# Performance work log

Measured on AMD Instinct MI355X. Metric: run time of the kernel, lower is better.

The kernel has to match this reference:

```python
import jax, jax.numpy as jnp
import numpy as np
import math

K = 4          # wavelet polynomial order
C = 16         # channel multiplier
MODES = 64     # retained Fourier modes (alpha)
L_LEVEL = 0    # coarsest level
B_SZ, N_SZ = 32, 8192
CK = C * K


def _get_filter_legendre(k):
    """Pure-numpy port of get_filter(base='legendre', k): Alpert multiwavelet filters."""
    from numpy.polynomial import legendre as npleg
    Poly = np.polynomial.Polynomial
    phi_coeff = np.zeros((k, k))
    phi_2x_coeff = np.zeros((k, k))
    for ki in range(k):
        c = np.zeros(ki + 1); c[ki] = 1.0
        base = Poly(npleg.leg2poly(c))
        p1 = base(Poly([-1.0, 2.0])).coef
        p2 = base(Poly([-1.0, 4.0])).coef
        phi_coeff[ki, :len(p1)] = np.sqrt(2 * ki + 1) * p1
        phi_2x_coeff[ki, :len(p2)] = np.sqrt(2.0) * np.sqrt(2 * ki + 1) * p2

    def proj_half(a, b, upper):
        # integral of poly(a)*poly(b) over [0,0.5] (upper=False) or [0.5,1] (upper=True)
        prod = np.convolve(a, b)
        prod[np.abs(prod) < 1e-8] = 0.0
        n = np.arange(len(prod))
        w = ((1.0 - np.power(0.5, n + 1)) if upper else np.power(0.5, n + 1)) / (n + 1)
        return (prod * w).sum()

    psi1_coeff = np.zeros((k, k)); psi2_coeff = np.zeros((k, k))
    for ki in range(k):
        psi1_coeff[ki, :] = phi_2x_coeff[ki, :]
        for i in range(k):
            p = proj_half(phi_2x_coeff[ki, :ki + 1], phi_coeff[i, :i + 1], False)
            psi1_coeff[ki, :] -= p * phi_coeff[i, :]
            psi2_coeff[ki, :] -= p * phi_coeff[i, :]
        for j in range(ki):
            p = proj_half(phi_2x_coeff[ki, :ki + 1], psi1_coeff[j, :], False)
            psi1_coeff[ki, :] -= p * psi1_coeff[j, :]
            psi2_coeff[ki, :] -= p * psi2_coeff[j, :]
        norm1 = proj_half(psi1_coeff[ki, :], psi1_coeff[ki, :], False)
        norm2 = proj_half(psi2_coeff[ki, :], psi2_coeff[ki, :], True)
        nrm = np.sqrt(norm1 + norm2)
        psi1_coeff[ki, :] /= nrm; psi2_coeff[ki, :] /= nrm
        psi1_coeff[np.abs(psi1_coeff) < 1e-8] = 0.0
        psi2_coeff[np.abs(psi2_coeff) < 1e-8] = 0.0

    t, w = npleg.leggauss(k)
    x_m = (t + 1.0) / 2.0; wm = w / 2.0     # Gauss-Legendre on [0,1]
    pv = np.polynomial.polynomial.polyval
    phi = lambda i, x: pv(x, phi_coeff[i])
    def psi(i, x):
        m = (x <= 0.5).astype(np.float64)
        return pv(x, psi1_coeff[i]) * m + pv(x, psi2_coeff[i]) * (1 - m)
    H0 = np.zeros((k, k)); H1 = np.zeros((k, k)); G0 = np.zeros((k, k)); G1 = np.zeros((k, k))
    s2 = np.sqrt(2.0)
    for ki in range(k):
        for kpi in range(k):
            H0[ki, kpi] = (wm * phi(ki, x_m / 2) * phi(kpi, x_m)).sum() / s2
            G0[ki, kpi] = (wm * psi(ki, x_m / 2) * phi(kpi, x_m)).sum() / s2
            H1[ki, kpi] = (wm * phi(ki, (x_m + 1) / 2) * phi(kpi, x_m)).sum() / s2
            G1[ki, kpi] = (wm * psi(ki, (x_m + 1) / 2) * phi(kpi, x_m)).sum() / s2
    for M in (H0, H1, G0, G1):
        M[np.abs(M) < 1e-8] = 0.0
    return H0, H1, G0, G1


_H0, _H1, _G0, _G1 = _get_filter_legendre(K)
# PHI0 = PHI1 = I for legendre, so H0r = H0 etc.
EC_S = jnp.asarray(np.concatenate((_H0.T, _H1.T), axis=0), dtype=jnp.float32)  # [2k,k]
EC_D = jnp.asarray(np.concatenate((_G0.T, _G1.T), axis=0), dtype=jnp.float32)
RC_E = jnp.asarray(np.concatenate((_H0, _G0), axis=0), dtype=jnp.float32)
RC_O = jnp.asarray(np.concatenate((_H1, _G1), axis=0), dtype=jnp.float32)


def _skft(x, w_re, w_im):
    """sparseKernelFT1d: FFT, truncated per-mode complex matmul, inverse FFT."""
    B, N, c, k = x.shape
    w = w_re + 1j * w_im                                   # [ck, ck, modes]
    xf = jnp.fft.rfft(x.reshape(B, N, c * k), axis=1)       # [B, N//2+1, ck]
    l = min(w.shape[-1], N // 2 + 1)
    out = jnp.einsum('bxi,iox->bxo', xf[:, :l, :], w[:, :, :l])
    out_full = jnp.zeros((B, N // 2 + 1, c * k), dtype=out.dtype).at[:, :l, :].set(out)
    y = jnp.fft.irfft(out_full, n=N, axis=1)
    return y.reshape(B, N, c, k)


def _mwt_cz1d(x, wA_re, wA_im, wB_re, wB_im, wC_re, wC_im, t0_w, t0_b):
    B, N, c, k = x.shape
    ns = int(math.floor(math.log2(N)))
    Ud, Us = [], []
    for _ in range(ns - L_LEVEL):
        # wavelet_transform
        xa = jnp.concatenate([x[:, ::2], x[:, 1::2]], axis=-1)   # [B, N/2, c, 2k]
        d = xa @ EC_D
        x = xa @ EC_S
        Ud.append(_skft(d, wA_re, wA_im) + _skft(x, wB_re, wB_im))
        Us.append(_skft(d, wC_re, wC_im))
    x = x @ t0_w.T + t0_b                                        # T0 linear on last dim k
    for i in range(ns - 1 - L_LEVEL, -1, -1):
        x = x + Us[i]
        x = jnp.concatenate([x, Ud[i]], axis=-1)                 # [B, M, c, 2k]
        x_e = x @ RC_E
        x_o = x @ RC_O
        M = x_e.shape[1]
        # interleave even/odd along the length axis
        x = jnp.stack([x_e, x_o], axis=2).reshape(B, 2 * M, c, k)
    return x


def setup_inputs() -> dict:
    key = jax.random.key(0)
    ks = jax.random.split(key, 8)
    scale = 1.0 / (CK * CK)
    return {
        'x': jax.random.normal(ks[0], (B_SZ, N_SZ, C, K), dtype=jnp.float32),
        'wA_re': scale * jax.random.uniform(ks[1], (CK, CK, MODES), dtype=jnp.float32),
        'wA_im': scale * jax.random.uniform(ks[2], (CK, CK, MODES), dtype=jnp.float32),
        'wB_re': scale * jax.random.uniform(ks[3], (CK, CK, MODES), dtype=jnp.float32),
        'wB_im': scale * jax.random.uniform(ks[4], (CK, CK, MODES), dtype=jnp.float32),
        'wC_re': scale * jax.random.uniform(ks[5], (CK, CK, MODES), dtype=jnp.float32),
        'wC_im': scale * jax.random.uniform(ks[6], (CK, CK, MODES), dtype=jnp.float32),
        't0_w': jax.random.normal(ks[7], (K, K), dtype=jnp.float32) / np.sqrt(K).astype(np.float32),
        't0_b': jnp.zeros((K,), dtype=jnp.float32),
    }


def reference(x, wA_re, wA_im, wB_re, wB_im, wC_re, wC_im, t0_w, t0_b):
    return _mwt_cz1d(x, wA_re, wA_im, wB_re, wB_im, wC_re, wC_im, t0_w, t0_b)
```

## Files before the change

### kernel.cpp

```cpp
#include <hip/hip_runtime.h>
#include <cmath>
#include <cstdint>


typedef __attribute__((ext_vector_type(8))) short bf16x8;
typedef __attribute__((ext_vector_type(4))) float f32x4;

struct Mat84 { float v[8][4]; };
struct Ptrs6 { const float* src[6]; uint16_t* dst[6]; };
struct TwLvls {
  int blkOff[14]; int Nl[13]; int l[13];
  unsigned long long fOff[13]; unsigned long long iOff[13];
};
struct FwdLvls {
  int blkOff[14]; int K[13]; int Kchunk[13];
  unsigned long long fOff[13]; unsigned long long bOff[13]; unsigned long long dOff[13];
};
struct MidLvls {
  int blkOff[14]; int l[13]; int nz[13];
  unsigned long long dOff[13]; unsigned long long sOff[13];
};
struct InvLvls {
  int blkOff[14]; int Nl[13]; int K2l[13];
  unsigned long long iOff[13]; unsigned long long sOff[13]; unsigned long long uOff[13];
};
struct DeepD { unsigned long long dsbOff[13]; };
struct DeepR { unsigned long long uOff[13]; };

__device__ __host__ inline uint16_t f2bf(float f) {
  union { float f; uint32_t u; } cv; cv.f = f;
  uint32_t u = cv.u;
  return (uint16_t)((u + 0x7fffu + ((u >> 16) & 1u)) >> 16);
}
__device__ inline float bf2f(uint16_t h) { return __uint_as_float((uint32_t)h << 16); }
__device__ inline uint32_t pack2(float a, float b) {
  return (uint32_t)f2bf(a) | ((uint32_t)f2bf(b) << 16);
}
__device__ inline bf16x8 negbf(bf16x8 x) {
  bf16x8 r;
#pragma unroll
  for (int j = 0; j < 8; j++) r[j] = (short)(x[j] ^ (short)0x8000);
  return r;
}
__device__ inline void gld_lds16(const uint16_t* g, uint16_t* l) {
  __builtin_amdgcn_global_load_lds(
      (const __attribute__((address_space(1))) void*)g,
      (__attribute__((address_space(3))) void*)l, 16, 0, 0);
}

static double proj_half_h(const double* a, const double* b, bool upper) {
  double prod[7] = {0, 0, 0, 0, 0, 0, 0};
  for (int i = 0; i < 4; i++)
    for (int j = 0; j < 4; j++)
      prod[i + j] += a[i] * b[j];
  for (int n = 0; n < 7; n++)
    if (fabs(prod[n]) < 1e-8) prod[n] = 0.0;
  double s = 0.0;
  for (int n = 0; n < 7; n++) {
    double w = upper ? (1.0 - pow(0.5, n + 1)) / (n + 1) : pow(0.5, n + 1) / (n + 1);
    s += prod[n] * w;
  }
  return s;
}
static double polyval4(const double* c, double x) {
  return c[0] + x * (c[1] + x * (c[2] + x * c[3]));
}

static void compute_filters(Mat84& ecs, Mat84& ecd, Mat84& rce, Mat84& rco) {
  const double leg[4][4] = {{1, 0, 0, 0}, {0, 1, 0, 0}, {-0.5, 0, 1.5, 0}, {0, -1.5, 0, 2.5}};
  double phi_c[4][4] = {}, phi2x_c[4][4] = {};
  const double s2 = sqrt(2.0);
  for (int ki = 0; ki < 4; ki++) {
    double a[4] = {0, 0, 0, 0};
    for (int j = 3; j >= 0; j--) {
      double na[4];
      for (int t = 0; t < 4; t++) { double v = -a[t]; if (t > 0) v += 2.0 * a[t - 1]; na[t] = v; }
      na[0] += leg[ki][j];
      for (int t = 0; t < 4; t++) a[t] = na[t];
    }
    for (int t = 0; t < 4; t++) phi_c[ki][t] = sqrt(2.0 * ki + 1.0) * a[t];
    double bb[4] = {0, 0, 0, 0};
    for (int j = 3; j >= 0; j--) {
      double nb[4];
      for (int t = 0; t < 4; t++) { double v = -bb[t]; if (t > 0) v += 4.0 * bb[t - 1]; nb[t] = v; }
      nb[0] += leg[ki][j];
      for (int t = 0; t < 4; t++) bb[t] = nb[t];
    }
    for (int t = 0; t < 4; t++) phi2x_c[ki][t] = s2 * sqrt(2.0 * ki + 1.0) * bb[t];
  }
  double psi1[4][4] = {}, psi2[4][4] = {};
  for (int ki = 0; ki < 4; ki++) {
    for (int t = 0; t < 4; t++) { psi1[ki][t] = phi2x_c[ki][t]; psi2[ki][t] = 0.0; }
    for (int i = 0; i < 4; i++) {
      double p = proj_half_h(phi2x_c[ki], phi_c[i], false);
      for (int t = 0; t < 4; t++) { psi1[ki][t] -= p * phi_c[i][t]; psi2[ki][t] -= p * phi_c[i][t]; }
    }
    for (int j = 0; j < ki; j++) {
      double p = proj_half_h(phi2x_c[ki], psi1[j], false);
      for (int t = 0; t < 4; t++) { psi1[ki][t] -= p * psi1[j][t]; psi2[ki][t] -= p * psi2[j][t]; }
    }
    double n1 = proj_half_h(psi1[ki], psi1[ki], false);
    double n2 = proj_half_h(psi2[ki], psi2[ki], true);
    double nr = sqrt(n1 + n2);
    for (int t = 0; t < 4; t++) { psi1[ki][t] /= nr; psi2[ki][t] /= nr; }
    for (int t = 0; t < 4; t++) {
      if (fabs(psi1[ki][t]) < 1e-8) psi1[ki][t] = 0.0;
      if (fabs(psi2[ki][t]) < 1e-8) psi2[ki][t] = 0.0;
    }
  }
  const double tq[4] = {-0.8611363115940526, -0.3399810435848563,
                        0.3399810435848563, 0.8611363115940526};
  const double wq[4] = {0.34785484513745385, 0.6521451548625461,
                        0.6521451548625461, 0.34785484513745385};
  double H0[4][4], H1[4][4], G0[4][4], G1[4][4];
  for (int ki = 0; ki < 4; ki++)
    for (int kp = 0; kp < 4; kp++) {
      double h0 = 0, h1 = 0, g0 = 0, g1 = 0;
      for (int m = 0; m < 4; m++) {
        double xm = (tq[m] + 1.0) * 0.5, wm = wq[m] * 0.5;
        double pk = polyval4(phi_c[kp], xm);
        h0 += wm * polyval4(phi_c[ki], xm * 0.5) * pk;
        h1 += wm * polyval4(phi_c[ki], (xm + 1.0) * 0.5) * pk;
        g0 += wm * polyval4(psi1[ki], xm * 0.5) * pk;
        g1 += wm * polyval4(psi2[ki], (xm + 1.0) * 0.5) * pk;
      }
      H0[ki][kp] = h0 / s2; H1[ki][kp] = h1 / s2; G0[ki][kp] = g0 / s2; G1[ki][kp] = g1 / s2;
    }
  for (int i = 0; i < 4; i++)
    for (int j = 0; j < 4; j++) {
      if (fabs(H0[i][j]) < 1e-8) H0[i][j] = 0.0;
      if (fabs(H1[i][j]) < 1e-8) H1[i][j] = 0.0;
      if (fabs(G0[i][j]) < 1e-8) G0[i][j] = 0.0;
      if (fabs(G1[i][j]) < 1e-8) G1[i][j] = 0.0;
    }
  for (int j = 0; j < 4; j++)
    for (int kk = 0; kk < 4; kk++) {
      ecs.v[j][kk]     = (float)H0[kk][j];
      ecs.v[j + 4][kk] = (float)H1[kk][j];
      ecd.v[j][kk]     = (float)G0[kk][j];
      ecd.v[j + 4][kk] = (float)G1[kk][j];
      rce.v[j][kk]     = (float)H0[j][kk];
      rce.v[j + 4][kk] = (float)G0[j][kk];
      rco.v[j][kk]     = (float)H1[j][kk];
      rco.v[j + 4][kk] = (float)G1[j][kk];
    }
}


__global__ void transpose_w(Ptrs6 p) {
  __shared__ float tile[64][65];
  int o = blockIdx.x, a = blockIdx.y;
  const float* w = p.src[a];
  uint16_t* wt = p.dst[a];
  int mm = threadIdx.x & 63, irow = threadIdx.x >> 6;
  for (int i = irow; i < 64; i += 4) tile[i][mm] = w[(((size_t)i * 64 + o) << 6) + mm];
  __syncthreads();
  int ii = threadIdx.x & 63, mrow = threadIdx.x >> 6;
  for (int mq = mrow; mq < 64; mq += 4)
    wt[(((size_t)mq * 64 + o) << 6) + ii] = f2bf(tile[ii][mq]);
}

__global__ void twiddle_all(uint16_t* __restrict__ FtwB, uint16_t* __restrict__ ItwB,
                            TwLvls tw) {
  int bx = blockIdx.x;
  int L = 0;
  while (L < 12 && bx >= tw.blkOff[L + 1]) L++;
  int Nl = tw.Nl[L], l = tw.l[L];
  int idx = (bx - tw.blkOff[L]) * 256 + threadIdx.x;
  if (idx >= 128 * Nl) return;
  uint16_t* Ftw = FtwB + tw.fOff[L];
  uint16_t* Itw = ItwB + tw.iOff[L];
  int n = idx % Nl, mm = idx / Nl;
  int m = (mm < l) ? mm : mm - l;
  int t = (m * n) & (Nl - 1);
  float ang = 6.2831853071795864769f * ((float)t / (float)Nl);
  float s, c;
  sincosf(ang, &s, &c);
  float fv = 0.f, iv = 0.f;
  float cm = (m == 0 || 2 * m == Nl) ? 1.0f : 2.0f;
  float sc = cm / (float)Nl;
  if (mm < l)          { fv = c;  iv = sc * c; }
  else if (mm < 2 * l) { fv = -s; iv = -sc * s; }
  Ftw[(size_t)mm * Nl + n] = f2bf(fv);
  Itw[(size_t)n * 128 + mm] = f2bf(iv);
}

__global__ __launch_bounds__(256) void decompose_kernel(
    const float* __restrict__ xin, float* __restrict__ s32,
    uint16_t* __restrict__ dsbfT, int Nl,
    Mat84 ecd, Mat84 ecs) {
  __shared__ uint32_t lds[128 * 34];
  int tid = threadIdx.x;
  int tile0 = blockIdx.x * 64;
  int b = blockIdx.y;
  int ci = tid & 15, nl = tid >> 4;
  float dall[4][4], sall[4][4];
#pragma unroll
  for (int jj = 0; jj < 4; jj++) {
    int n = tile0 + nl * 4 + jj;
    const float* r0 = xin + ((size_t)(b * 2 * Nl + 2 * n)) * 64 + ci * 4;
    float4 xe = *(const float4*)r0;
    float4 xo = *(const float4*)(r0 + 64);
    float xa[8] = {xe.x, xe.y, xe.z, xe.w, xo.x, xo.y, xo.z, xo.w};
    float d[4] = {0, 0, 0, 0}, s[4] = {0, 0, 0, 0};
#pragma unroll
    for (int j = 0; j < 8; j++) {
      float v = xa[j];
#pragma unroll
      for (int kk = 0; kk < 4; kk++) {
        d[kk] = fmaf(v, ecd.v[j][kk], d[kk]);
        s[kk] = fmaf(v, ecs.v[j][kk], s[kk]);
      }
    }
    *(float4*)&s32[((size_t)b * Nl + n) * 64 + ci * 4] = make_float4(s[0], s[1], s[2], s[3]);
#pragma unroll
    for (int kk = 0; kk < 4; kk++) { dall[jj][kk] = d[kk]; sall[jj][kk] = s[kk]; }
  }
#pragma unroll
  for (int kk = 0; kk < 4; kk++) {
    uint32_t d01 = pack2(dall[0][kk], dall[1][kk]);
    uint32_t d23 = pack2(dall[2][kk], dall[3][kk]);
    uint32_t s01 = pack2(sall[0][kk], sall[1][kk]);
    uint32_t s23 = pack2(sall[2][kk], sall[3][kk]);
    int cd = ci * 4 + kk;
    *(uint2*)&lds[cd * 34 + nl * 2] = make_uint2(d01, d23);
    *(uint2*)&lds[(64 + cd) * 34 + nl * 2] = make_uint2(s01, s23);
  }
  __syncthreads();
  uint32_t* outu = (uint32_t*)dsbfT;
  for (int e = tid; e < 128 * 32; e += 256) {
    int col = e >> 5, u = e & 31;
    uint32_t v = lds[col * 34 + u];
    outu[((((size_t)b * 128 + col) * Nl + tile0) >> 1) + u] = v;
  }
}

__global__ __launch_bounds__(256) void dec_deep(const float* __restrict__ sIn,
                                                uint16_t* __restrict__ DSbf,
                                                float* __restrict__ sFin,
                                                DeepD dd, Mat84 ecd, Mat84 ecs) {
  __shared__ float bufA[512 * 17];
  __shared__ float bufB[256 * 17];
  __shared__ uint16_t stg[32 * 256];
  int tid = threadIdx.x;
  int b = blockIdx.x >> 2, cc = blockIdx.x & 3;
  for (int e = tid; e < 512 * 4; e += 256) {
    int n = e >> 2, f4 = e & 3;
    float4 v = *(const float4*)&sIn[((size_t)b * 512 + n) * 64 + cc * 16 + f4 * 4];
    bufA[n * 17 + f4 * 4 + 0] = v.x;
    bufA[n * 17 + f4 * 4 + 1] = v.y;
    bufA[n * 17 + f4 * 4 + 2] = v.z;
    bufA[n * 17 + f4 * 4 + 3] = v.w;
  }
  __syncthreads();
  float* cur = bufA;
  float* nxt = bufB;
  int len = 512;
  for (int L = 4; L <= 12; L++) {
    int M = len >> 1;
    for (int e = tid; e < M * 4; e += 256) {
      int n = e >> 2, cl = e & 3;
      float xa[8];
#pragma unroll
      for (int j = 0; j < 4; j++) {
        xa[j]     = cur[(2 * n) * 17 + cl * 4 + j];
        xa[4 + j] = cur[(2 * n + 1) * 17 + cl * 4 + j];
      }
      float d[4] = {0, 0, 0, 0}, s[4] = {0, 0, 0, 0};
#pragma unroll
      for (int j = 0; j < 8; j++) {
        float v = xa[j];
#pragma unroll
        for (int kk = 0; kk < 4; kk++) {
          d[kk] = fmaf(v, ecd.v[j][kk], d[kk]);
          s[kk] = fmaf(v, ecs.v[j][kk], s[kk]);
        }
      }
#pragma unroll
      for (int kk = 0; kk < 4; kk++) {
        nxt[n * 17 + cl * 4 + kk] = s[kk];
        stg[(cl * 4 + kk) * 256 + n] = f2bf(d[kk]);
        stg[(16 + cl * 4 + kk) * 256 + n] = f2bf(s[kk]);
      }
    }
    __syncthreads();
    uint16_t* out = DSbf + dd.dsbOff[L];
    if (M >= 2) {
      int M2 = M >> 1;
      int lg = 31 - __builtin_clz(M2);
      uint32_t* outu = (uint32_t*)out;
      const uint32_t* stgu = (const uint32_t*)stg;
      for (int e = tid; e < 32 * M2; e += 256) {
        int r = e >> lg, u = e & (M2 - 1);
        int grow = (r < 16) ? (cc * 16 + r) : (64 + cc * 16 + (r - 16));
        outu[(((size_t)b * 128 + grow) * M >> 1) + u] = stgu[r * 128 + u];
      }
    } else {
      for (int e = tid; e < 32; e += 256) {
        int grow = (e < 16) ? (cc * 16 + e) : (64 + cc * 16 + (e - 16));
        out[(size_t)b * 128 + grow] = stg[e * 256];
      }
    }
    __syncthreads();
    float* t = cur; cur = nxt; nxt = t;
    len = M;
  }
  for (int e = tid; e < 16; e += 256) sFin[(size_t)b * 64 + cc * 16 + e] = cur[e];
}

__global__ __launch_bounds__(256) void fwd_all(const uint16_t* __restrict__ FtwB,
                                               const uint16_t* __restrict__ DSbfB,
                                               float* __restrict__ DfsB, FwdLvls fl) {
  __shared__ uint16_t As[2][4096];
  __shared__ uint16_t Bs[2][4096];
  int bx = blockIdx.x, L = 0;
  while (L < 12 && bx >= fl.blkOff[L + 1]) L++;
  int local = bx - fl.blkOff[L];
  int b = local & 31, z = local >> 5;
  int K = fl.K[L];
  int k0 = z * fl.Kchunk[L];
  int k1 = k0 + fl.Kchunk[L]; if (k1 > K) k1 = K;
  const uint16_t* A = FtwB + fl.fOff[L];
  const uint16_t* Bb = DSbfB + fl.bOff[L] + (size_t)b * 128 * K;
  int tid = threadIdx.x;
  int w = tid >> 6, lane = tid & 63;
  int wr = w >> 1, wc = w & 1;
  int lr = lane & 15, q = lane >> 4;
  f32x4 acc[4][4];
#pragma unroll
  for (int i = 0; i < 4; i++)
#pragma unroll
    for (int j = 0; j < 4; j++) acc[i][j] = (f32x4){0.f, 0.f, 0.f, 0.f};

  if (K >= 32) {
    int rsub = lane >> 2, g = lane & 3;
    int nsteps = (k1 - k0) >> 5;
    auto stage = [&](int buf, int kc) {
#pragma unroll
      for (int j = 0; j < 2; ++j) {
        int c = w * 2 + j;
        int row = c * 16 + rsub;
        int gs = (g ^ ((row >> 1) & 3)) << 3;
        gld_lds16(A + (size_t)row * K + kc + gs, &As[buf][c * 512]);
        gld_lds16(Bb + (size_t)row * K + kc + gs, &Bs[buf][c * 512]);
      }
    };
    stage(0, k0);
    __syncthreads();
    int cur = 0;
    int sw = (lr >> 1) & 3;
    for (int s = 0; s < nsteps; ++s) {
      if (s + 1 < nsteps) stage(cur ^ 1, k0 + ((s + 1) << 5));
      bf16x8 af[4], bfv[4];
#pragma unroll
      for (int t = 0; t < 4; t++) {
        af[t]  = *(const bf16x8*)&As[cur][(wr * 64 + t * 16 + lr) * 32 + ((q ^ sw) << 3)];
        bfv[t] = *(const bf16x8*)&Bs[cur][(wc * 64 + t * 16 + lr) * 32 + ((q ^ sw) << 3)];
      }
#pragma unroll
      for (int mt = 0; mt < 4; mt++)
#pragma unroll
        for (int nt = 0; nt < 4; nt++)
          acc[mt][nt] = __builtin_amdgcn_mfma_f32_16x16x32_bf16(af[mt], bfv[nt], acc[mt][nt], 0, 0, 0);
      __syncthreads();
      cur ^= 1;
    }
  } else {
    for (int s = tid; s < 512; s += 256) {
      int row = s >> 2, k8 = (s & 3) * 8;
      uint16_t ta[8], tb[8];
#pragma unroll
      for (int j = 0; j < 8; j++) {
        ta[j] = (k8 + j < k1) ? A[(size_t)row * K + k8 + j] : (uint16_t)0;
        tb[j] = (k8 + j < k1) ? Bb[(size_t)row * K + k8 + j] : (uint16_t)0;
      }
      *(uint4*)&As[0][row * 32 + k8] = *(const uint4*)ta;
      *(uint4*)&Bs[0][row * 32 + k8] = *(const uint4*)tb;
    }
    __syncthreads();
    bf16x8 af[4], bfv[4];
#pragma unroll
    for (int t = 0; t < 4; t++) {
      af[t]  = *(const bf16x8*)&As[0][(wr * 64 + t * 16 + lr) * 32 + q * 8];
      bfv[t] = *(const bf16x8*)&Bs[0][(wc * 64 + t * 16 + lr) * 32 + q * 8];
    }
#pragma unroll
    for (int mt = 0; mt < 4; mt++)
#pragma unroll
      for (int nt = 0; nt < 4; nt++)
        acc[mt][nt] = __builtin_amdgcn_mfma_f32_16x16x32_bf16(af[mt], bfv[nt], acc[mt][nt], 0, 0, 0);
  }

  float* Cb = DfsB + fl.dOff[L] + ((size_t)z * 32 + b) * 16384;
#pragma unroll
  for (int mt = 0; mt < 4; mt++) {
    int row0 = wr * 64 + mt * 16 + q * 4;
#pragma unroll
    for (int nt = 0; nt < 4; nt++) {
      int col = wc * 64 + nt * 16 + lr;
#pragma unroll
      for (int r = 0; r < 4; r++)
        Cb[(size_t)(row0 + r) * 128 + col] = acc[mt][nt][r];
    }
  }
}

__global__ __launch_bounds__(256) void middle_all(
    const float* __restrict__ DfsB,
    const uint16_t* __restrict__ wAr, const uint16_t* __restrict__ wAi,
    const uint16_t* __restrict__ wBr, const uint16_t* __restrict__ wBi,
    const uint16_t* __restrict__ wCr, const uint16_t* __restrict__ wCi,
    uint16_t* __restrict__ SpecTB, MidLvls ml) {
  __shared__ uint16_t Bs[6 * 64 * 64];
  __shared__ uint16_t As[8 * 32 * 64];
  int bx = blockIdx.x, L = 0;
  while (L < 12 && bx >= ml.blkOff[L + 1]) L++;
  int m = bx - ml.blkOff[L];
  int l = ml.l[L], nz = ml.nz[L];
  const float* Dfs = DfsB + ml.dOff[L];
  uint16_t* SpecT = SpecTB + ml.sOff[L];
  int tid = threadIdx.x;

#pragma unroll
  for (int a = 0; a < 6; a++) {
    const uint16_t* wpa = (a == 0) ? wAr : (a == 1) ? wAi : (a == 2) ? wBr
                        : (a == 3) ? wBi : (a == 4) ? wCr : wCi;
#pragma unroll
    for (int t0 = 0; t0 < 512; t0 += 256) {
      int t = t0 + tid;
      int o = t >> 3, g = t & 7;
      uint4 v = *(const uint4*)&wpa[(((size_t)m * 64 + o) << 6) + (g << 3)];
      *(uint4*)((char*)Bs + a * 8192 + o * 128 + (((g ^ (o & 7)) << 4))) = v;
    }
  }
  for (int e = tid; e < 2048; e += 256) {
    int c4 = (e & 31) * 4, r = (e >> 5) & 1, bb = e >> 6;
    size_t row = r ? (size_t)(l + m) : (size_t)m;
    float4 s = make_float4(0.f, 0.f, 0.f, 0.f);
    for (int z = 0; z < nz; z++) {
      float4 v = *(const float4*)&Dfs[((((size_t)z * 32 + bb) * 128 + row) << 7) + c4];
      s.x += v.x; s.y += v.y; s.z += v.z; s.w += v.w;
    }
    int vec = r + ((c4 >= 64) ? 2 : 0);
    int i0 = c4 & 63;
    float f[4] = {s.x, s.y, s.z, s.w};
    uint16_t hi[4], lo[4];
#pragma unroll
    for (int j = 0; j < 4; j++) {
      hi[j] = f2bf(f[j]);
      lo[j] = f2bf(f[j] - bf2f(hi[j]));
    }
    int g = i0 >> 3, w8 = (i0 & 7) * 2;
    char* ph = (char*)As + ((vec * 2 + 0) * 32 + bb) * 128 + ((g ^ (bb & 7)) << 4) + w8;
    char* pl = (char*)As + ((vec * 2 + 1) * 32 + bb) * 128 + ((g ^ (bb & 7)) << 4) + w8;
    *(uint2*)ph = make_uint2((uint32_t)hi[0] | ((uint32_t)hi[1] << 16),
                             (uint32_t)hi[2] | ((uint32_t)hi[3] << 16));
    *(uint2*)pl = make_uint2((uint32_t)lo[0] | ((uint32_t)lo[1] << 16),
                             (uint32_t)lo[2] | ((uint32_t)lo[3] << 16));
  }
  __syncthreads();

  int w = tid >> 6, lane = tid & 63;
  int lr = lane & 15, q = lane >> 4;
  f32x4 acc[2][4];
#pragma unroll
  for (int i = 0; i < 2; i++)
#pragma unroll
    for (int j = 0; j < 4; j++) acc[i][j] = (f32x4){0.f, 0.f, 0.f, 0.f};

  auto combo = [&](int v, int a, int ng) {
    bf16x8 bf[4][2];
#pragma unroll
    for (int nt = 0; nt < 4; nt++) {
      int o = nt * 16 + lr;
#pragma unroll
      for (int ks = 0; ks < 2; ks++) {
        int g = ks * 4 + q;
        bf[nt][ks] = *(const bf16x8*)((const char*)Bs + a * 8192 + o * 128 +
                                      ((g ^ (o & 7)) << 4));
      }
    }
#pragma unroll
    for (int p = 0; p < 2; p++) {
#pragma unroll
      for (int mt = 0; mt < 2; mt++) {
        int bb = mt * 16 + lr;
        const char* ab = (const char*)As + ((v * 2 + p) * 32 + bb) * 128;
        bf16x8 a0 = *(const bf16x8*)(ab + (((0 + q) ^ (bb & 7)) << 4));
        bf16x8 a1 = *(const bf16x8*)(ab + (((4 + q) ^ (bb & 7)) << 4));
        if (ng) { a0 = negbf(a0); a1 = negbf(a1); }
#pragma unroll
        for (int nt = 0; nt < 4; nt++) {
          acc[mt][nt] = __builtin_amdgcn_mfma_f32_16x16x32_bf16(a0, bf[nt][0], acc[mt][nt], 0, 0, 0);
          acc[mt][nt] = __builtin_amdgcn_mfma_f32_16x16x32_bf16(a1, bf[nt][1], acc[mt][nt], 0, 0, 0);
        }
      }
    }
  };
  if (w == 0) {
    combo(0, 0, 0); combo(1, 1, 1); combo(2, 2, 0); combo(3, 3, 1);
  } else if (w == 1) {
    combo(1, 0, 0); combo(0, 1, 0); combo(3, 2, 0); combo(2, 3, 0);
  } else if (w == 2) {
    combo(0, 4, 0); combo(1, 5, 1);
  } else {
    combo(1, 4, 0); combo(0, 5, 0);
  }

  int krow = (w & 1) ? (l + m) : m;
  int colbase = (w >= 2) ? 64 : 0;
#pragma unroll
  for (int mt = 0; mt < 2; mt++) {
#pragma unroll
    for (int nt = 0; nt < 4; nt++) {
#pragma unroll
      for (int r = 0; r < 4; r++) {
        int bb = mt * 16 + q * 4 + r;
        int oo = nt * 16 + lr;
        SpecT[((size_t)bb * 128 + colbase + oo) * 128 + krow] = f2bf(acc[mt][nt][r]);
      }
    }
  }
}

__global__ __launch_bounds__(256) void inv_all(const uint16_t* __restrict__ ItwB,
                                               const uint16_t* __restrict__ SpecTB,
                                               uint16_t* __restrict__ UdB,
                                               uint16_t* __restrict__ UsB, InvLvls il) {
  __shared__ uint16_t lds[32768];
  int bx = blockIdx.x, L = 0;
  while (L < 12 && bx >= il.blkOff[L + 1]) L++;
  int local = bx - il.blkOff[L];
  int b = local & 31, n0 = (local >> 5) * 128;
  int Nl = il.Nl[L], K2l = il.K2l[L];
  const uint16_t* A = ItwB + il.iOff[L];
  const uint16_t* Bb = SpecTB + il.sOff[L] + (size_t)b * 128 * 128;
  uint16_t* Ud = UdB + il.uOff[L];
  uint16_t* Us = UsB + il.uOff[L];
  int tid = threadIdx.x;
  int w = tid >> 6, lane = tid & 63;
  int wr = w >> 1, wc = w & 1;
  int lr = lane & 15, q = lane >> 4;
  f32x4 acc[4][4];
#pragma unroll
  for (int i = 0; i < 4; i++)
#pragma unroll
    for (int j = 0; j < 4; j++) acc[i][j] = (f32x4){0.f, 0.f, 0.f, 0.f};

  if (K2l == 128) {
    uint16_t* As0 = lds;
    uint16_t* Bs0 = lds + 16384;
    int rsub = lane >> 4, p = lane & 15;
#pragma unroll
    for (int i = 0; i < 8; i++) {
      int rowb = w * 32 + i * 4;
      int row = rowb + rsub;
      int gs = (p ^ (row & 7)) << 3;
      gld_lds16(A + (size_t)(n0 + row) * 128 + gs, As0 + rowb * 128);
      gld_lds16(Bb + (size_t)row * 128 + gs, Bs0 + rowb * 128);
    }
    __syncthreads();
    int sw = lr & 7;
#pragma unroll
    for (int kc = 0; kc < 4; kc++) {
      bf16x8 af[4], bfv[4];
#pragma unroll
      for (int t = 0; t < 4; t++) {
        int g = kc * 4 + q;
        af[t]  = *(const bf16x8*)&As0[(wr * 64 + t * 16 + lr) * 128 + ((g ^ sw) << 3)];
        bfv[t] = *(const bf16x8*)&Bs0[(wc * 64 + t * 16 + lr) * 128 + ((g ^ sw) << 3)];
      }
#pragma unroll
      for (int mt = 0; mt < 4; mt++)
#pragma unroll
        for (int nt = 0; nt < 4; nt++)
          acc[mt][nt] = __builtin_amdgcn_mfma_f32_16x16x32_bf16(af[mt], bfv[nt], acc[mt][nt], 0, 0, 0);
    }
    __syncthreads();
#pragma unroll
    for (int mt = 0; mt < 4; mt++)
#pragma unroll
      for (int nt = 0; nt < 4; nt++)
#pragma unroll
        for (int r = 0; r < 4; r++)
          lds[(wr * 64 + mt * 16 + q * 4 + r) * 132 + wc * 64 + nt * 16 + lr] =
              f2bf(acc[mt][nt][r]);
    __syncthreads();
    uint16_t* Udb = Ud + ((size_t)b * Nl + n0) * 64;
    uint16_t* Usb = Us + ((size_t)b * Nl + n0) * 64;
#pragma unroll
    for (int i = 0; i < 4; i++) {
      int f = i * 256 + tid;
      int row = f >> 3, c8 = (f & 7) * 8;
      *(uint4*)(Udb + (size_t)f * 8) = *(const uint4*)&lds[row * 132 + c8];
      *(uint4*)(Usb + (size_t)f * 8) = *(const uint4*)&lds[row * 132 + 64 + c8];
    }
    return;
  }

  uint16_t* As0 = lds;
  uint16_t* Bs0 = lds + 4096;
  for (int kc = 0; kc < 128; kc += 32) {
    for (int s = tid; s < 512; s += 256) {
      int row = s >> 2, k8 = (s & 3) * 8;
      int kg = kc + k8;
      *(uint4*)&As0[row * 32 + k8] = *(const uint4*)&A[((size_t)(n0 + row)) * 128 + kg];
      uint16_t tb[8];
      if (kg + 8 <= K2l) {
        *(uint4*)tb = *(const uint4*)&Bb[(size_t)row * 128 + kg];
      } else {
#pragma unroll
        for (int j = 0; j < 8; j++)
          tb[j] = (kg + j < K2l) ? Bb[(size_t)row * 128 + kg + j] : (uint16_t)0;
      }
      *(uint4*)&Bs0[row * 32 + k8] = *(const uint4*)tb;
    }
    __syncthreads();
    bf16x8 af[4], bfv[4];
#pragma unroll
    for (int t = 0; t < 4; t++) {
      af[t]  = *(const bf16x8*)&As0[(wr * 64 + t * 16 + lr) * 32 + q * 8];
      bfv[t] = *(const bf16x8*)&Bs0[(wc * 64 + t * 16 + lr) * 32 + q * 8];
    }
#pragma unroll
    for (int mt = 0; mt < 4; mt++)
#pragma unroll
      for (int nt = 0; nt < 4; nt++)
        acc[mt][nt] = __builtin_amdgcn_mfma_f32_16x16x32_bf16(af[mt], bfv[nt], acc[mt][nt], 0, 0, 0);
    __syncthreads();
  }
#pragma unroll
  for (int mt = 0; mt < 4; mt++) {
    int row0 = wr * 64 + mt * 16 + q * 4;
#pragma unroll
    for (int nt = 0; nt < 4; nt++) {
      int col = wc * 64 + nt * 16 + lr;
#pragma unroll
      for (int r = 0; r < 4; r++) {
        int n = n0 + row0 + r;
        if (n < Nl) {
          uint16_t v = f2bf(acc[mt][nt][r]);
          if (col < 64) Ud[((size_t)b * Nl + n) * 64 + col] = v;
          else          Us[((size_t)b * Nl + n) * 64 + (col - 64)] = v;
        }
      }
    }
  }
}

__global__ __launch_bounds__(256) void recon_deep(const float* __restrict__ sFin,
                                                  const float* __restrict__ t0w,
                                                  const float* __restrict__ t0b,
                                                  const uint16_t* __restrict__ UdB,
                                                  const uint16_t* __restrict__ UsB,
                                                  float* __restrict__ xOut,
                                                  DeepR rl, Mat84 rce, Mat84 rco) {
  __shared__ float bufA[512 * 17];
  __shared__ float bufB[256 * 17];
  int tid = threadIdx.x;
  int b = blockIdx.x >> 2, cc = blockIdx.x & 3;
  if (tid < 16) {
    int cl = tid >> 2, kk = tid & 3;
    const float* sp = sFin + (size_t)b * 64 + cc * 16 + cl * 4;
    float v = t0b[kk];
#pragma unroll
    for (int k2 = 0; k2 < 4; k2++) v += t0w[kk * 4 + k2] * sp[k2];
    bufB[cl * 4 + kk] = v;
  }
  __syncthreads();
  float* cur = bufB;
  float* nxt = bufA;
  int M = 1;
  for (int i = 12; i >= 4; i--) {
    const uint16_t* Ud = UdB + rl.uOff[i];
    const uint16_t* Us = UsB + rl.uOff[i];
    for (int e = tid; e < M * 4; e += 256) {
      int n = e >> 2, cl = e & 3;
      size_t ua = ((size_t)b * M + n) * 64 + cc * 16 + cl * 4;
      ushort4 uu = *(const ushort4*)&Us[ua];
      ushort4 dd = *(const ushort4*)&Ud[ua];
      float t[8];
      t[0] = cur[n * 17 + cl * 4 + 0] + bf2f(uu.x);
      t[1] = cur[n * 17 + cl * 4 + 1] + bf2f(uu.y);
      t[2] = cur[n * 17 + cl * 4 + 2] + bf2f(uu.z);
      t[3] = cur[n * 17 + cl * 4 + 3] + bf2f(uu.w);
      t[4] = bf2f(dd.x); t[5] = bf2f(dd.y); t[6] = bf2f(dd.z); t[7] = bf2f(dd.w);
      float ev[4] = {0, 0, 0, 0}, ov[4] = {0, 0, 0, 0};
#pragma unroll
      for (int j = 0; j < 8; j++) {
        float v = t[j];
#pragma unroll
        for (int kk = 0; kk < 4; kk++) {
          ev[kk] = fmaf(v, rce.v[j][kk], ev[kk]);
          ov[kk] = fmaf(v, rco.v[j][kk], ov[kk]);
        }
      }
#pragma unroll
      for (int kk = 0; kk < 4; kk++) {
        nxt[(2 * n) * 17 + cl * 4 + kk] = ev[kk];
        nxt[(2 * n + 1) * 17 + cl * 4 + kk] = ov[kk];
      }
    }
    __syncthreads();
    float* t = cur; cur = nxt; nxt = t;
    M <<= 1;
  }
  for (int e = tid; e < 512 * 4; e += 256) {
    int n = e >> 2, f4 = e & 3;
    float4 v = make_float4(cur[n * 17 + f4 * 4 + 0], cur[n * 17 + f4 * 4 + 1],
                           cur[n * 17 + f4 * 4 + 2], cur[n * 17 + f4 * 4 + 3]);
    *(float4*)&xOut[((size_t)b * 512 + n) * 64 + cc * 16 + f4 * 4] = v;
  }
}

__global__ void recon_kernel(const float* __restrict__ x, const uint16_t* __restrict__ Ud,
                             const uint16_t* __restrict__ Us, float* __restrict__ out,
                             int M, int lgM, Mat84 rce, Mat84 rco) {
  int idx = blockIdx.x * 256 + threadIdx.x;
  int ci = idx & 15;
  int nb = idx >> 4;
  int m = nb & (M - 1);
  int b = nb >> lgM;
  if (b >= 32) return;
  size_t basei = ((size_t)b * M + m) * 64 + ci * 4;
  float4 xv = *(const float4*)&x[basei];
  ushort4 uu = *(const ushort4*)&Us[basei];
  ushort4 dd = *(const ushort4*)&Ud[basei];
  float t[8] = {xv.x + bf2f(uu.x), xv.y + bf2f(uu.y), xv.z + bf2f(uu.z), xv.w + bf2f(uu.w),
                bf2f(dd.x), bf2f(dd.y), bf2f(dd.z), bf2f(dd.w)};
  float e[4] = {0, 0, 0, 0}, o[4] = {0, 0, 0, 0};
#pragma unroll
  for (int j = 0; j < 8; j++) {
    float v = t[j];
#pragma unroll
    for (int kk = 0; kk < 4; kk++) {
      e[kk] = fmaf(v, rce.v[j][kk], e[kk]);
      o[kk] = fmaf(v, rco.v[j][kk], o[kk]);
    }
  }
  size_t ob = ((size_t)b * 2 * M + 2 * m) * 64 + ci * 4;
  *(float4*)&out[ob] = make_float4(e[0], e[1], e[2], e[3]);
  *(float4*)&out[ob + 64] = make_float4(o[0], o[1], o[2], o[3]);
}

extern "C" void kernel_launch(void* const* d_in, const int* in_sizes, int n_in,
                              void* d_out, int out_size, void* d_ws, size_t ws_size,
                              hipStream_t stream) {
  const float* x_in = (const float*)d_in[0];
  const float* t0w = (const float*)d_in[7];
  const float* t0b = (const float*)d_in[8];

  Mat84 ECS, ECD, RCE, RCO;
  compute_filters(ECS, ECD, RCE, RCO);

  int NlA[13], lA[13], nzA[13], KchA[13];
  size_t fOff[13], iOff[13], uOffA[13], dsbOff[13], dOff[13], sOff[13];
  size_t fo = 0, io = 0, uo = 0, db = 0, df = 0;
  for (int L = 0; L < 13; L++) {
    int Nl = 8192 >> (L + 1);
    int l = Nl / 2 + 1; if (l > 64) l = 64;
    NlA[L] = Nl; lA[L] = l;
    nzA[L] = (L == 0) ? 4 : (L == 1) ? 2 : 1;
    KchA[L] = Nl / nzA[L];
    fOff[L] = fo; fo += (size_t)128 * Nl;
    iOff[L] = io; io += (size_t)Nl * 128;
    uOffA[L] = uo; uo += (size_t)32 * 64 * Nl;
    dsbOff[L] = db; db += (size_t)32 * 128 * Nl;
    dOff[L] = df; df += (size_t)nzA[L] * 32 * 128 * 128;
    sOff[L] = (size_t)L * 32 * 128 * 128;
  }
  io += 128 * 128;

  char* base = (char*)d_ws;
  size_t off = 0;
  auto alloc = [&](size_t bytes) -> char* {
    char* p = base + off;
    off += (bytes + 255) & ~(size_t)255;
    return p;
  };
  float*    SA    = (float*)alloc((size_t)32 * 4096 * 64 * 4);
  float*    SB    = (float*)alloc((size_t)32 * 2048 * 64 * 4);
  float*    SC    = (float*)alloc((size_t)32 * 1024 * 64 * 4);
  float*    SD    = (float*)alloc((size_t)32 * 512 * 64 * 4);
  float*    SFin  = (float*)alloc((size_t)32 * 64 * 4);
  uint16_t* Ud    = (uint16_t*)alloc(uo * 2);
  uint16_t* Us    = (uint16_t*)alloc(uo * 2);
  float*    Dfs   = (float*)alloc(df * 4);
  uint16_t* SpecT = (uint16_t*)alloc((size_t)13 * 32 * 128 * 128 * 2);
  uint16_t* DSbf  = (uint16_t*)alloc(db * 2);
  uint16_t* Ftw   = (uint16_t*)alloc(fo * 2);
  uint16_t* Itw   = (uint16_t*)alloc(io * 2);
  uint16_t* wT[6];
  for (int a = 0; a < 6; a++) wT[a] = (uint16_t*)alloc((size_t)64 * 64 * 64 * 2);

  Ptrs6 p6;
  for (int a = 0; a < 6; a++) { p6.src[a] = (const float*)d_in[1 + a]; p6.dst[a] = wT[a]; }
  transpose_w<<<dim3(64, 6), 256, 0, stream>>>(p6);

  TwLvls tw;
  int bo = 0;
  for (int L = 0; L < 13; L++) {
    tw.blkOff[L] = bo;
    bo += (128 * NlA[L] + 255) / 256;
    tw.Nl[L] = NlA[L]; tw.l[L] = lA[L];
    tw.fOff[L] = fOff[L]; tw.iOff[L] = iOff[L];
  }
  tw.blkOff[13] = bo;
  twiddle_all<<<bo, 256, 0, stream>>>(Ftw, Itw, tw);

  {
    const float* srcs[4] = {x_in, SA, SB, SC};
    float* dsts[4] = {SA, SB, SC, SD};
    for (int L = 0; L < 4; L++) {
      int Nl = NlA[L];
      decompose_kernel<<<dim3(Nl / 64, 32), 256, 0, stream>>>(srcs[L], dsts[L],
                                                              DSbf + dsbOff[L], Nl, ECD, ECS);
    }
  }

  DeepD dd;
  for (int L = 0; L < 13; L++) dd.dsbOff[L] = dsbOff[L];
  dec_deep<<<128, 256, 0, stream>>>(SD, DSbf, SFin, dd, ECD, ECS);

  FwdLvls fl;
  bo = 0;
  for (int L = 0; L < 13; L++) {
    fl.blkOff[L] = bo; bo += 32 * nzA[L];
    fl.K[L] = NlA[L]; fl.Kchunk[L] = KchA[L];
    fl.fOff[L] = fOff[L]; fl.bOff[L] = dsbOff[L]; fl.dOff[L] = dOff[L];
  }
  fl.blkOff[13] = bo;
  fwd_all<<<bo, 256, 0, stream>>>(Ftw, DSbf, Dfs, fl);

  MidLvls ml;
  bo = 0;
  for (int L = 0; L < 13; L++) {
    ml.blkOff[L] = bo; bo += lA[L];
    ml.l[L] = lA[L]; ml.nz[L] = nzA[L];
    ml.dOff[L] = dOff[L]; ml.sOff[L] = sOff[L];
  }
  ml.blkOff[13] = bo;
  middle_all<<<bo, 256, 0, stream>>>(Dfs, wT[0], wT[1], wT[2], wT[3], wT[4], wT[5], SpecT, ml);

  InvLvls il;
  bo = 0;
  for (int L = 0; L < 13; L++) {
    il.blkOff[L] = bo; bo += ((NlA[L] + 127) / 128) * 32;
    il.Nl[L] = NlA[L]; il.K2l[L] = 2 * lA[L];
    il.iOff[L] = iOff[L]; il.sOff[L] = sOff[L]; il.uOff[L] = uOffA[L];
  }
  il.blkOff[13] = bo;
  inv_all<<<bo, 256, 0, stream>>>(Itw, SpecT, Ud, Us, il);

  DeepR rl;
  for (int L = 0; L < 13; L++) rl.uOff[L] = uOffA[L];
  recon_deep<<<128, 256, 0, stream>>>(SFin, t0w, t0b, Ud, Us, SD, rl, RCE, RCO);

  {
    float* xs[4] = {SD, SC, SB, SA};
    float* outs[4] = {SC, SB, SA, (float*)d_out};
    for (int t = 0; t < 4; t++) {
      int i = 3 - t;
      int M = NlA[i];
      int lg = 31 - __builtin_clz(M);
      recon_kernel<<<M * 2, 256, 0, stream>>>(xs[t], Ud + uOffA[i], Us + uOffA[i], outs[t],
                                              M, lg, RCE, RCO);
    }
  }
}
```

Baseline: 331.4 us.

## Fuse first four decompose and reconstruct levels into single LDS-resident kernels

Replaces four per-level decompose launches with one kernel that reads a 512-sample tile per channel group and runs levels 0-3 in shared memory. It likewise replaces four per-level reconstruct launches with one kernel that walks levels 3 down to 0 in shared memory before writing the output. This drops the fp32 intermediate buffers SA/SB/SC and their global round-trips, and cuts six launches. The cost is lower per-block parallelism in the deeper levels (fewer active threads per iteration) and narrower 16-channel-slice memory accesses.

```diff
diff --git a/kernel.cpp b/kernel.cpp
--- a/kernel.cpp
+++ b/kernel.cpp
@@ -185,53 +185,98 @@
   Itw[(size_t)n * 128 + mm] = f2bf(iv);
 }
 
-__global__ __launch_bounds__(256) void decompose_kernel(
-    const float* __restrict__ xin, float* __restrict__ s32,
-    uint16_t* __restrict__ dsbfT, int Nl,
-    Mat84 ecd, Mat84 ecs) {
-  __shared__ uint32_t lds[128 * 34];
+__global__ __launch_bounds__(256) void dec_fused(const float* __restrict__ xin,
+                                                 uint16_t* __restrict__ DSbf,
+                                                 float* __restrict__ sOut,
+                                                 DeepD dd, Mat84 ecd, Mat84 ecs) {
+  __shared__ float bufA[256 * 17];
+  __shared__ float bufB[128 * 17];
+  __shared__ uint16_t stg[32 * 256];
   int tid = threadIdx.x;
-  int tile0 = blockIdx.x * 64;
-  int b = blockIdx.y;
-  int ci = tid & 15, nl = tid >> 4;
-  float dall[4][4], sall[4][4];
-#pragma unroll
-  for (int jj = 0; jj < 4; jj++) {
-    int n = tile0 + nl * 4 + jj;
-    const float* r0 = xin + ((size_t)(b * 2 * Nl + 2 * n)) * 64 + ci * 4;
-    float4 xe = *(const float4*)r0;
-    float4 xo = *(const float4*)(r0 + 64);
-    float xa[8] = {xe.x, xe.y, xe.z, xe.w, xo.x, xo.y, xo.z, xo.w};
-    float d[4] = {0, 0, 0, 0}, s[4] = {0, 0, 0, 0};
-#pragma unroll
-    for (int j = 0; j < 8; j++) {
-      float v = xa[j];
+  int bx = blockIdx.x;
+  int t = bx & 15, cc = (bx >> 4) & 3, b = bx >> 6;
+
+  {
+    int nbase = t * 256;
+    for (int e = tid; e < 1024; e += 256) {
+      int n = e >> 2, lci = e & 3;
+      const float* r0 = xin + ((size_t)b * 8192 + 2 * (nbase + n)) * 64 + cc * 16 + lci * 4;
+      float4 xe = *(const float4*)r0;
+      float4 xo = *(const float4*)(r0 + 64);
+      float xa[8] = {xe.x, xe.y, xe.z, xe.w, xo.x, xo.y, xo.z, xo.w};
+      float d[4] = {0, 0, 0, 0}, s[4] = {0, 0, 0, 0};
+#pragma unroll
+      for (int j = 0; j < 8; j++) {
+        float v = xa[j];
+#pragma unroll
+        for (int kk = 0; kk < 4; kk++) {
+          d[kk] = fmaf(v, ecd.v[j][kk], d[kk]);
+          s[kk] = fmaf(v, ecs.v[j][kk], s[kk]);
+        }
+      }
 #pragma unroll
       for (int kk = 0; kk < 4; kk++) {
-        d[kk] = fmaf(v, ecd.v[j][kk], d[kk]);
-        s[kk] = fmaf(v, ecs.v[j][kk], s[kk]);
-      }
-    }
-    *(float4*)&s32[((size_t)b * Nl + n) * 64 + ci * 4] = make_float4(s[0], s[1], s[2], s[3]);
-#pragma unroll
-    for (int kk = 0; kk < 4; kk++) { dall[jj][kk] = d[kk]; sall[jj][kk] = s[kk]; }
-  }
-#pragma unroll
-  for (int kk = 0; kk < 4; kk++) {
-    uint32_t d01 = pack2(dall[0][kk], dall[1][kk]);
-    uint32_t d23 = pack2(dall[2][kk], dall[3][kk]);
-    uint32_t s01 = pack2(sall[0][kk], sall[1][kk]);
-    uint32_t s23 = pack2(sall[2][kk], sall[3][kk]);
-    int cd = ci * 4 + kk;
-    *(uint2*)&lds[cd * 34 + nl * 2] = make_uint2(d01, d23);
-    *(uint2*)&lds[(64 + cd) * 34 + nl * 2] = make_uint2(s01, s23);
-  }
-  __syncthreads();
-  uint32_t* outu = (uint32_t*)dsbfT;
-  for (int e = tid; e < 128 * 32; e += 256) {
-    int col = e >> 5, u = e & 31;
-    uint32_t v = lds[col * 34 + u];
-    outu[((((size_t)b * 128 + col) * Nl + tile0) >> 1) + u] = v;
+        bufA[n * 17 + lci * 4 + kk] = s[kk];
+        stg[(lci * 4 + kk) * 256 + n] = f2bf(d[kk]);
+        stg[(16 + lci * 4 + kk) * 256 + n] = f2bf(s[kk]);
+      }
+    }
+    __syncthreads();
+    uint32_t* outu = (uint32_t*)(DSbf + dd.dsbOff[0]);
+    const uint32_t* stgu = (const uint32_t*)stg;
+    for (int e = tid; e < 32 * 128; e += 256) {
+      int r = e >> 7, u = e & 127;
+      int grow = (r < 16) ? (cc * 16 + r) : (64 + cc * 16 + (r - 16));
+      outu[((((size_t)b * 128 + grow) * 4096 + nbase) >> 1) + u] = stgu[r * 128 + u];
+    }
+    __syncthreads();
+  }
+  float* cur = bufA;
+  float* nxt = bufB;
+  int M = 128;
+  for (int Lev = 1; Lev <= 3; Lev++) {
+    int nbase = t * M;
+    int Nl = 4096 >> Lev;
+    for (int e = tid; e < M * 4; e += 256) {
+      int n = e >> 2, lci = e & 3;
+      float xa[8];
+#pragma unroll
+      for (int j = 0; j < 4; j++) {
+        xa[j]     = cur[(2 * n) * 17 + lci * 4 + j];
+        xa[4 + j] = cur[(2 * n + 1) * 17 + lci * 4 + j];
+      }
+      float d[4] = {0, 0, 0, 0}, s[4] = {0, 0, 0, 0};
+#pragma unroll
+      for (int j = 0; j < 8; j++) {
+        float v = xa[j];
+#pragma unroll
+        for (int kk = 0; kk < 4; kk++) {
+          d[kk] = fmaf(v, ecd.v[j][kk], d[kk]);
+          s[kk] = fmaf(v, ecs.v[j][kk], s[kk]);
+        }
+      }
+#pragma unroll
+      for (int kk = 0; kk < 4; kk++) {
+        if (Lev < 3) nxt[n * 17 + lci * 4 + kk] = s[kk];
+        stg[(lci * 4 + kk) * 256 + n] = f2bf(d[kk]);
+        stg[(16 + lci * 4 + kk) * 256 + n] = f2bf(s[kk]);
+      }
+      if (Lev == 3)
+        *(float4*)&sOut[((size_t)b * 512 + nbase + n) * 64 + cc * 16 + lci * 4] =
+            make_float4(s[0], s[1], s[2], s[3]);
+    }
+    __syncthreads();
+    int cols = M >> 1, lg = 31 - __builtin_clz(cols);
+    uint32_t* outu = (uint32_t*)(DSbf + dd.dsbOff[Lev]);
+    const uint32_t* stgu = (const uint32_t*)stg;
+    for (int e = tid; e < 32 * cols; e += 256) {
+      int r = e >> lg, u = e & (cols - 1);
+      int grow = (r < 16) ? (cc * 16 + r) : (64 + cc * 16 + (r - 16));
+      outu[((((size_t)b * 128 + grow) * Nl + nbase) >> 1) + u] = stgu[r * 128 + u];
+    }
+    __syncthreads();
+    float* tmp = cur; cur = nxt; nxt = tmp;
+    M >>= 1;
   }
 }
 
@@ -713,34 +758,92 @@
   }
 }
 
-__global__ void recon_kernel(const float* __restrict__ x, const uint16_t* __restrict__ Ud,
-                             const uint16_t* __restrict__ Us, float* __restrict__ out,
-                             int M, int lgM, Mat84 rce, Mat84 rco) {
-  int idx = blockIdx.x * 256 + threadIdx.x;
-  int ci = idx & 15;
-  int nb = idx >> 4;
-  int m = nb & (M - 1);
-  int b = nb >> lgM;
-  if (b >= 32) return;
-  size_t basei = ((size_t)b * M + m) * 64 + ci * 4;
-  float4 xv = *(const float4*)&x[basei];
-  ushort4 uu = *(const ushort4*)&Us[basei];
-  ushort4 dd = *(const ushort4*)&Ud[basei];
-  float t[8] = {xv.x + bf2f(uu.x), xv.y + bf2f(uu.y), xv.z + bf2f(uu.z), xv.w + bf2f(uu.w),
-                bf2f(dd.x), bf2f(dd.y), bf2f(dd.z), bf2f(dd.w)};
-  float e[4] = {0, 0, 0, 0}, o[4] = {0, 0, 0, 0};
-#pragma unroll
-  for (int j = 0; j < 8; j++) {
-    float v = t[j];
-#pragma unroll
-    for (int kk = 0; kk < 4; kk++) {
-      e[kk] = fmaf(v, rce.v[j][kk], e[kk]);
-      o[kk] = fmaf(v, rco.v[j][kk], o[kk]);
-    }
-  }
-  size_t ob = ((size_t)b * 2 * M + 2 * m) * 64 + ci * 4;
-  *(float4*)&out[ob] = make_float4(e[0], e[1], e[2], e[3]);
-  *(float4*)&out[ob + 64] = make_float4(o[0], o[1], o[2], o[3]);
+__global__ __launch_bounds__(256) void recon_fused(const float* __restrict__ xin,
+                                                   const uint16_t* __restrict__ UdB,
+                                                   const uint16_t* __restrict__ UsB,
+                                                   float* __restrict__ out,
+                                                   DeepR rl, Mat84 rce, Mat84 rco) {
+  __shared__ float bufA[256 * 17];
+  __shared__ float bufB[256 * 17];
+  int tid = threadIdx.x;
+  int bx = blockIdx.x;
+  int t = bx & 15, cc = (bx >> 4) & 3, b = bx >> 6;
+
+  {
+    int nbase = t * 32;
+    const uint16_t* Ud = UdB + rl.uOff[3];
+    const uint16_t* Us = UsB + rl.uOff[3];
+    for (int e = tid; e < 128; e += 256) {
+      int n = e >> 2, lci = e & 3;
+      size_t ua = ((size_t)b * 512 + nbase + n) * 64 + cc * 16 + lci * 4;
+      float4 xv = *(const float4*)&xin[ua];
+      ushort4 uu = *(const ushort4*)&Us[ua];
+      ushort4 dd = *(const ushort4*)&Ud[ua];
+      float tv[8] = {xv.x + bf2f(uu.x), xv.y + bf2f(uu.y), xv.z + bf2f(uu.z),
+                     xv.w + bf2f(uu.w), bf2f(dd.x), bf2f(dd.y), bf2f(dd.z), bf2f(dd.w)};
+      float ev[4] = {0, 0, 0, 0}, ov[4] = {0, 0, 0, 0};
+#pragma unroll
+      for (int j = 0; j < 8; j++) {
+        float v = tv[j];
+#pragma unroll
+        for (int kk = 0; kk < 4; kk++) {
+          ev[kk] = fmaf(v, rce.v[j][kk], ev[kk]);
+          ov[kk] = fmaf(v, rco.v[j][kk], ov[kk]);
+        }
+      }
+#pragma unroll
+      for (int kk = 0; kk < 4; kk++) {
+        bufA[(2 * n) * 17 + lci * 4 + kk] = ev[kk];
+        bufA[(2 * n + 1) * 17 + lci * 4 + kk] = ov[kk];
+      }
+    }
+    __syncthreads();
+  }
+  float* cur = bufA;
+  float* nxt = bufB;
+  int m = 64;
+  for (int i = 2; i >= 0; i--) {
+    int Mlev = 8192 >> (i + 1);
+    int nbase = t * m;
+    const uint16_t* Ud = UdB + rl.uOff[i];
+    const uint16_t* Us = UsB + rl.uOff[i];
+    for (int e = tid; e < m * 4; e += 256) {
+      int n = e >> 2, lci = e & 3;
+      size_t ua = ((size_t)b * Mlev + nbase + n) * 64 + cc * 16 + lci * 4;
+      ushort4 uu = *(const ushort4*)&Us[ua];
+      ushort4 dd = *(const ushort4*)&Ud[ua];
+      float tv[8];
+      tv[0] = cur[n * 17 + lci * 4 + 0] + bf2f(uu.x);
+      tv[1] = cur[n * 17 + lci * 4 + 1] + bf2f(uu.y);
+      tv[2] = cur[n * 17 + lci * 4 + 2] + bf2f(uu.z);
+      tv[3] = cur[n * 17 + lci * 4 + 3] + bf2f(uu.w);
+      tv[4] = bf2f(dd.x); tv[5] = bf2f(dd.y); tv[6] = bf2f(dd.z); tv[7] = bf2f(dd.w);
+      float ev[4] = {0, 0, 0, 0}, ov[4] = {0, 0, 0, 0};
+#pragma unroll
+      for (int j = 0; j < 8; j++) {
+        float v = tv[j];
+#pragma unroll
+        for (int kk = 0; kk < 4; kk++) {
+          ev[kk] = fmaf(v, rce.v[j][kk], ev[kk]);
+          ov[kk] = fmaf(v, rco.v[j][kk], ov[kk]);
+        }
+      }
+      if (i > 0) {
+#pragma unroll
+        for (int kk = 0; kk < 4; kk++) {
+          nxt[(2 * n) * 17 + lci * 4 + kk] = ev[kk];
+          nxt[(2 * n + 1) * 17 + lci * 4 + kk] = ov[kk];
+        }
+      } else {
+        size_t ob = ((size_t)b * 8192 + 2 * (nbase + n)) * 64 + cc * 16 + lci * 4;
+        *(float4*)&out[ob] = make_float4(ev[0], ev[1], ev[2], ev[3]);
+        *(float4*)&out[ob + 64] = make_float4(ov[0], ov[1], ov[2], ov[3]);
+      }
+    }
+    __syncthreads();
+    float* tmp = cur; cur = nxt; nxt = tmp;
+    m <<= 1;
+  }
 }
 
 extern "C" void kernel_launch(void* const* d_in, const int* in_sizes, int n_in,
@@ -778,9 +881,6 @@
     off += (bytes + 255) & ~(size_t)255;
     return p;
   };
-  float*    SA    = (float*)alloc((size_t)32 * 4096 * 64 * 4);
-  float*    SB    = (float*)alloc((size_t)32 * 2048 * 64 * 4);
-  float*    SC    = (float*)alloc((size_t)32 * 1024 * 64 * 4);
   float*    SD    = (float*)alloc((size_t)32 * 512 * 64 * 4);
   float*    SFin  = (float*)alloc((size_t)32 * 64 * 4);
   uint16_t* Ud    = (uint16_t*)alloc(uo * 2);
@@ -808,18 +908,11 @@
   tw.blkOff[13] = bo;
   twiddle_all<<<bo, 256, 0, stream>>>(Ftw, Itw, tw);
 
-  {
-    const float* srcs[4] = {x_in, SA, SB, SC};
-    float* dsts[4] = {SA, SB, SC, SD};
-    for (int L = 0; L < 4; L++) {
-      int Nl = NlA[L];
-      decompose_kernel<<<dim3(Nl / 64, 32), 256, 0, stream>>>(srcs[L], dsts[L],
-                                                              DSbf + dsbOff[L], Nl, ECD, ECS);
-    }
-  }
-
   DeepD dd;
   for (int L = 0; L < 13; L++) dd.dsbOff[L] = dsbOff[L];
+
+  dec_fused<<<2048, 256, 0, stream>>>(x_in, DSbf, SD, dd, ECD, ECS);
+
   dec_deep<<<128, 256, 0, stream>>>(SD, DSbf, SFin, dd, ECD, ECS);
 
   FwdLvls fl;
@@ -854,17 +947,8 @@
 
   DeepR rl;
   for (int L = 0; L < 13; L++) rl.uOff[L] = uOffA[L];
+
   recon_deep<<<128, 256, 0, stream>>>(SFin, t0w, t0b, Ud, Us, SD, rl, RCE, RCO);
 
-  {
-    float* xs[4] = {SD, SC, SB, SA};
-    float* outs[4] = {SC, SB, SA, (float*)d_out};
-    for (int t = 0; t < 4; t++) {
-      int i = 3 - t;
-      int M = NlA[i];
-      int lg = 31 - __builtin_clz(M);
-      recon_kernel<<<M * 2, 256, 0, stream>>>(xs[t], Ud + uOffA[i], Us + uOffA[i], outs[t],
-                                              M, lg, RCE, RCO);
-    }
-  }
-}
+  recon_fused<<<2048, 256, 0, stream>>>(SD, Ud, Us, (float*)d_out, rl, RCE, RCO);
+}
```

Result: faster. 290.8 us (-12.3%).
